# Kernel tuning notes

Hardware: AMD Instinct MI355X
Metric: run time of the kernel (lower is better)

## Reference

```python
import jax, jax.numpy as jnp
import numpy as np


def setup_inputs() -> dict:
    key = jax.random.key(0)
    ks = jax.random.split(key, 7)
    B, D, d1, d2, d3 = 256, 256, 1024, 512, 256
    s = lambda f: 1.0 / np.sqrt(f)  # torch nn.Linear-style init scale
    return {
        "x": jax.random.normal(ks[0], (B, D), jnp.float32),
        "W1": jax.random.normal(ks[1], (d1, D), jnp.float32) * s(D),
        "b1": jax.random.normal(ks[2], (d1,), jnp.float32) * s(D),
        "W2": jax.random.normal(ks[3], (d2, d1), jnp.float32) * s(d1),
        "b2": jax.random.normal(ks[4], (d2,), jnp.float32) * s(d1),
        "W3": jax.random.normal(ks[5], (d3, d2), jnp.float32) * s(d2),
        "b3": jax.random.normal(ks[6], (d3,), jnp.float32) * s(d2),
        "k": 10,
    }


def _border_dists(x, W1, b1, W2, b2, W3, b3):
    # Layer 1: pre-activations and boundary distances. For the first layer the
    # effective linear map is W1 itself (shared across the batch).
    z1 = x @ W1.T + b1                                   # [B, d1]
    dist1 = jnp.abs(z1) / jnp.linalg.norm(W1, axis=1)    # [B, d1]
    m1 = (z1 > 0).astype(x.dtype)
    V1 = m1[:, :, None] * W1[None]                       # [B, d1, D] per-instance map after ReLU
    h1 = m1 * z1

    # Layer 2
    z2 = h1 @ W2.T + b2                                  # [B, d2]
    V2 = jnp.einsum('oi,bid->bod', W2, V1)               # [B, d2, D]
    dist2 = jnp.abs(z2) / jnp.linalg.norm(V2, axis=2)
    m2 = (z2 > 0).astype(x.dtype)
    h2 = m2 * z2

    # Layer 3
    z3 = h2 @ W3.T + b3                                  # [B, d3]
    V3 = jnp.einsum('oi,bid->bod', W3, m2[:, :, None] * V2)  # [B, d3, D]
    dist3 = jnp.abs(z3) / jnp.linalg.norm(V3, axis=2)

    return jnp.concatenate([dist1, dist2, dist3], axis=1)  # [B, d1+d2+d3]


def reference(x, W1, b1, W2, b2, W3, b3, k):
    dists = _border_dists(x, W1, b1, W2, b2, W3, b3)
    # smallest-k distances per instance via top_k on negated distances
    neg_top, _ = jax.lax.top_k(-dists, k)                # [B, k]
    return jnp.sum(-neg_top)                             # border-distance loss (scalar)
```

## Files before the change

kernel.cpp:

```cpp
#include <hip/hip_runtime.h>
#include <math.h>
#include <float.h>

#define B   256
#define D   256
#define D1  1024
#define D2  512
#define D3  256
#define NDIST (D1 + D2 + D3)
#define CQ  2.0f

typedef __attribute__((ext_vector_type(8))) short short8;
typedef __attribute__((ext_vector_type(4))) float f32x4;
typedef __attribute__((ext_vector_type(4))) int   i32x4;

__device__ __forceinline__ float waveReduceSum(float v) {
    #pragma unroll
    for (int off = 32; off > 0; off >>= 1)
        v += __shfl_down(v, off, 64);
    return v;
}
__device__ __forceinline__ float waveReduceMax(float v) {
    #pragma unroll
    for (int off = 32; off > 0; off >>= 1)
        v = fmaxf(v, __shfl_down(v, off, 64));
    return v;
}
__device__ __forceinline__ unsigned short f2bf(float f) {
    unsigned int u = __float_as_uint(f);
    u = (u + 0x7FFFu + ((u >> 16) & 1u)) >> 16;
    return (unsigned short)u;
}
__device__ __forceinline__ float bf2f(unsigned short h) {
    return __uint_as_float(((unsigned int)h) << 16);
}
__device__ __forceinline__ void gld16(const void* g, void* l) {
    __builtin_amdgcn_global_load_lds(
        (const __attribute__((address_space(1))) unsigned int*)g,
        (__attribute__((address_space(3))) unsigned int*)l, 16, 0, 0);
}
__device__ __forceinline__ int swz_src(int row, int lane) {
    return ((lane & 3) + ((row >> 1) & 3)) & 3;
}
__device__ __forceinline__ int swz_frag(int row, int quad) {
    return row * 32 + (((quad - ((row >> 1) & 3)) & 3) * 8);
}

__device__ __forceinline__ void split_job(const float* src, unsigned short* hi,
                                          unsigned short* lo, int off) {
    float4 v = *(const float4*)(src + off);
    ushort4 h, l;
    h.x = f2bf(v.x); l.x = f2bf(v.x - bf2f(h.x));
    h.y = f2bf(v.y); l.y = f2bf(v.y - bf2f(h.y));
    h.z = f2bf(v.z); l.z = f2bf(v.z - bf2f(h.z));
    h.w = f2bf(v.w); l.w = f2bf(v.w - bf2f(h.w));
    *(ushort4*)(hi + off) = h;
    *(ushort4*)(lo + off) = l;
}

__device__ __forceinline__ void split8(const float* p, short8& h8, short8& l8) {
    float4 a = *(const float4*)(p);
    float4 b = *(const float4*)(p + 4);
    float hv[8] = { a.x, a.y, a.z, a.w, b.x, b.y, b.z, b.w };
    #pragma unroll
    for (int q = 0; q < 8; q++) {
        unsigned short hh = f2bf(hv[q]);
        h8[q] = (short)hh;
        l8[q] = (short)f2bf(hv[q] - bf2f(hh));
    }
}

template <int KD, int KL>
__device__ __forceinline__ void mfma3_64(
    const unsigned short* __restrict__ Ahi, const unsigned short* __restrict__ Alo,
    const unsigned short* __restrict__ Bhi, const unsigned short* __restrict__ Blo,
    int m0, int n0, int k0, unsigned short* sm, f32x4 acc[2][2]) {
    int tid = threadIdx.x;
    int l = tid & 63, w = tid >> 6;
    int rsub = l >> 2;
    int quad = l >> 4, l16 = l & 15;
    int wm = (w >> 1) * 32, wn = (w & 1) * 32;
    unsigned short* sAh = sm;
    unsigned short* sAl = sm + 2048;
    unsigned short* sBh = sm + 4096;
    unsigned short* sBl = sm + 6144;
    ptrdiff_t dA = Alo - Ahi, dB = Blo - Bhi;
    int rloc = w * 16 + rsub;
    int c = swz_src(rloc, l);
    const unsigned short* pa = Ahi + (size_t)(m0 + rloc) * KD + k0 + c * 8;
    const unsigned short* pb = Bhi + (size_t)(n0 + rloc) * KD + k0 + c * 8;
    int aoff[2], boff[2];
    #pragma unroll
    for (int mt = 0; mt < 2; mt++) aoff[mt] = swz_frag(wm + mt * 16 + l16, quad);
    #pragma unroll
    for (int nt = 0; nt < 2; nt++) boff[nt] = swz_frag(wn + nt * 16 + l16, quad);
    for (int kk = 0; kk < KL; kk += 32) {
        gld16(pa + kk,      sAh + w * 512);
        gld16(pa + dA + kk, sAl + w * 512);
        gld16(pb + kk,      sBh + w * 512);
        gld16(pb + dB + kk, sBl + w * 512);
        __syncthreads();
        short8 ah[2], al[2], bh[2], bl[2];
        #pragma unroll
        for (int mt = 0; mt < 2; mt++) {
            ah[mt] = *(const short8*)(sAh + aoff[mt]);
            al[mt] = *(const short8*)(sAl + aoff[mt]);
        }
        #pragma unroll
        for (int nt = 0; nt < 2; nt++) {
            bh[nt] = *(const short8*)(sBh + boff[nt]);
            bl[nt] = *(const short8*)(sBl + boff[nt]);
        }
        #pragma unroll
        for (int mt = 0; mt < 2; mt++)
            #pragma unroll
            for (int nt = 0; nt < 2; nt++) {
                acc[mt][nt] = __builtin_amdgcn_mfma_f32_16x16x32_bf16(ah[mt], bh[nt], acc[mt][nt], 0, 0, 0);
                acc[mt][nt] = __builtin_amdgcn_mfma_f32_16x16x32_bf16(ah[mt], bl[nt], acc[mt][nt], 0, 0, 0);
                acc[mt][nt] = __builtin_amdgcn_mfma_f32_16x16x32_bf16(al[mt], bh[nt], acc[mt][nt], 0, 0, 0);
            }
        __syncthreads();
    }
}

__global__ __launch_bounds__(256) void k_l1p(
    const float* __restrict__ x, const float* __restrict__ W1,
    const float* __restrict__ W2, const float* __restrict__ W3,
    const float* __restrict__ b1,
    float* __restrict__ dists, unsigned char* __restrict__ m1q,
    unsigned short* __restrict__ h1hi, unsigned short* __restrict__ h1lo,
    float* __restrict__ zeros, float* __restrict__ outp,
    unsigned short* __restrict__ W2hi, unsigned short* __restrict__ W2lo,
    unsigned short* __restrict__ W3hi, unsigned short* __restrict__ W3lo,
    signed char* __restrict__ W1Ti8, float* __restrict__ saq,
    signed char* __restrict__ W2i8,  float* __restrict__ sbq,
    signed char* __restrict__ W3i8,  float* __restrict__ s3q,
    float* __restrict__ rn1) {
    __shared__ __align__(16) unsigned short sm[8192];
    int blk = blockIdx.x;
    int t = threadIdx.x;

    if (blk < 64) {
        unsigned short* sAh = sm;
        unsigned short* sAl = sm + 2048;
        unsigned short* sBh = sm + 4096;
        unsigned short* sBl = sm + 6144;
        int m0 = (blk & 3) * 64, n0 = (blk >> 2) * 64;
        int l = t & 63, w = t >> 6;
        int rsub = l >> 2;
        int quad = l >> 4, l16 = l & 15;
        int wm = (w >> 1) * 32, wn = (w & 1) * 32;
        int rloc = w * 16 + rsub;
        int c = swz_src(rloc, l);
        const float* pax = x + (size_t)(m0 + rloc) * D + c * 8;
        const float* pbw = W1 + (size_t)(n0 + rloc) * D + c * 8;
        int aoff[2], boff[2];
        #pragma unroll
        for (int mt = 0; mt < 2; mt++) aoff[mt] = swz_frag(wm + mt * 16 + l16, quad);
        #pragma unroll
        for (int nt = 0; nt < 2; nt++) boff[nt] = swz_frag(wn + nt * 16 + l16, quad);
        int wrA = w * 512 + l * 8;
        f32x4 acc[2][2] = {};
        for (int kk = 0; kk < D; kk += 32) {
            short8 ha, la, hb, lb;
            split8(pax + kk, ha, la);
            split8(pbw + kk, hb, lb);
            *(short8*)(sAh + wrA) = ha;
            *(short8*)(sAl + wrA) = la;
            *(short8*)(sBh + wrA) = hb;
            *(short8*)(sBl + wrA) = lb;
            __syncthreads();
            short8 ah[2], al[2], bh[2], bl[2];
            #pragma unroll
            for (int mt = 0; mt < 2; mt++) {
                ah[mt] = *(const short8*)(sAh + aoff[mt]);
                al[mt] = *(const short8*)(sAl + aoff[mt]);
            }
            #pragma unroll
            for (int nt = 0; nt < 2; nt++) {
                bh[nt] = *(const short8*)(sBh + boff[nt]);
                bl[nt] = *(const short8*)(sBl + boff[nt]);
            }
            #pragma unroll
            for (int mt = 0; mt < 2; mt++)
                #pragma unroll
                for (int nt = 0; nt < 2; nt++) {
                    acc[mt][nt] = __builtin_amdgcn_mfma_f32_16x16x32_bf16(ah[mt], bh[nt], acc[mt][nt], 0, 0, 0);
                    acc[mt][nt] = __builtin_amdgcn_mfma_f32_16x16x32_bf16(ah[mt], bl[nt], acc[mt][nt], 0, 0, 0);
                    acc[mt][nt] = __builtin_amdgcn_mfma_f32_16x16x32_bf16(al[mt], bh[nt], acc[mt][nt], 0, 0, 0);
                }
            __syncthreads();
        }
        #pragma unroll
        for (int mt = 0; mt < 2; mt++)
            #pragma unroll
            for (int nt = 0; nt < 2; nt++) {
                int n = n0 + wn + nt * 16 + l16;
                float bv = b1[n];
                #pragma unroll
                for (int r = 0; r < 4; r++) {
                    int m = m0 + wm + mt * 16 + quad * 4 + r;
                    float z = acc[mt][nt][r] + bv;
                    size_t idx = (size_t)m * D1 + n;
                    dists[idx] = fabsf(z);
                    m1q[idx] = (z > 0.f) ? 0xFFu : 0u;
                    float h = z > 0.f ? z : 0.f;
                    unsigned short hh = f2bf(h);
                    h1hi[idx] = hh;
                    h1lo[idx] = f2bf(h - bf2f(hh));
                }
            }
        return;
    }
    if (blk < 448) {
        if (blk == 64 && t == 0) outp[0] = 0.f;
        int i4 = (blk - 64) * 1024 + t * 4;
        *(float4*)(zeros + i4) = make_float4(0.f, 0.f, 0.f, 0.f);
        return;
    }
    if (blk < 960) {
        split_job(W2, W2hi, W2lo, (blk - 448) * 1024 + t * 4);
        return;
    }
    if (blk < 1088) {
        split_job(W3, W3hi, W3lo, (blk - 960) * 1024 + t * 4);
        return;
    }
    if (blk < 1120) {
        int ty = t >> 5, tx = t & 31;
        int d = (blk - 1088) * 8 + ty;
        float m = 0.f;
        for (int i = tx; i < D1; i += 32) m = fmaxf(m, fabsf(W1[(size_t)i * D + d]));
        #pragma unroll
        for (int off = 16; off > 0; off >>= 1) m = fmaxf(m, __shfl_down(m, off, 32));
        m = __shfl(m, 0, 32);
        m = fmaxf(m, 1e-20f);
        if (tx == 0) saq[d] = m / 127.f;
        float inv = 127.f / m;
        for (int i = tx; i < D1; i += 32) {
            int q = __float2int_rn(W1[(size_t)i * D + d] * inv);
            W1Ti8[(size_t)d * D1 + i] = (signed char)q;
        }
        return;
    }
    if (blk < 1248) {
        int o = (blk - 1120) * 4 + (t >> 6);
        int l = t & 63;
        const float* row = W2 + (size_t)o * D1;
        float m = 0.f;
        for (int tt = l; tt < D1; tt += 64) m = fmaxf(m, fabsf(row[tt]));
        m = waveReduceMax(m);
        m = __shfl(m, 0, 64);
        m = fmaxf(m, 1e-20f);
        if (l == 0) sbq[o] = m / 127.f;
        float inv = 127.f / m;
        for (int tt = l; tt < D1; tt += 64)
            W2i8[(size_t)o * D1 + tt] = (signed char)__float2int_rn(row[tt] * inv);
        return;
    }
    if (blk < 1312) {
        int p = (blk - 1248) * 4 + (t >> 6);
        int l = t & 63;
        const float* row = W3 + (size_t)p * D2;
        float m = 0.f;
        for (int tt = l; tt < D2; tt += 64) m = fmaxf(m, fabsf(row[tt]));
        m = waveReduceMax(m);
        m = __shfl(m, 0, 64);
        m = fmaxf(m, 1e-20f);
        if (l == 0) s3q[p] = m / 127.f;
        float inv = 127.f / m;
        for (int tt = l; tt < D2; tt += 64)
            W3i8[(size_t)p * D2 + tt] = (signed char)__float2int_rn(row[tt] * inv);
        return;
    }
    {
        int gw = (blk - 1312) * 4 + (t >> 6);
        int lane = t & 63;
        const float* row = W1 + (size_t)gw * D;
        float s = 0.f;
        for (int tt = lane; tt < D; tt += 64) { float v = row[tt]; s += v * v; }
        s = waveReduceSum(s);
        if (lane == 0) rn1[gw] = sqrtf(s);
    }
}

__global__ __launch_bounds__(256, 2) void k_big1(
    const unsigned short* __restrict__ h1hi, const unsigned short* __restrict__ h1lo,
    const unsigned short* __restrict__ W2hi, const unsigned short* __restrict__ W2lo,
    float* __restrict__ z2,
    const signed char* __restrict__ W1Ti8,
    const signed char* __restrict__ W2i8,
    const unsigned char* __restrict__ m1q,
    const float* __restrict__ saq,
    const float* __restrict__ sbq,
    signed char* __restrict__ qV2,
    float* __restrict__ norm2) {
    __shared__ __align__(16) unsigned char smem[67584];
    int bid = blockIdx.x;

    if (bid < 128) {
        unsigned short* sm = (unsigned short*)smem;
        int m0 = (bid & 3) * 64, n0 = ((bid >> 2) & 7) * 64, k0 = (bid >> 5) * 256;
        f32x4 acc[2][2] = {};
        mfma3_64<D1, 256>(h1hi, h1lo, W2hi, W2lo, m0, n0, k0, sm, acc);
        int l = threadIdx.x & 63, w = threadIdx.x >> 6;
        int quad = l >> 4, l16 = l & 15;
        int wm = (w >> 1) * 32, wn = (w & 1) * 32;
        #pragma unroll
        for (int mt = 0; mt < 2; mt++)
            #pragma unroll
            for (int nt = 0; nt < 2; nt++) {
                int n = n0 + wn + nt * 16 + l16;
                #pragma unroll
                for (int r = 0; r < 4; r++) {
                    int m = m0 + wm + mt * 16 + quad * 4 + r;
                    atomicAdd(&z2[(size_t)m * D2 + n], acc[mt][nt][r]);
                }
            }
        return;
    }

    int j = bid - 128;
    int m0 = (j & 1) * 128;
    int o0 = ((j >> 1) & 3) * 128;
    int b0 = (j >> 3) * 2;
    int tid = threadIdx.x;
    int l = tid & 63, w = tid >> 6;
    int quad = l >> 4, l16 = l & 15;
    int wm = (w >> 1) * 64, wn = (w & 1) * 64;
    unsigned char* mbuf = (unsigned char*)smem + 65536;

    *(int2*)(mbuf + tid * 8) = *(const int2*)(m1q + (size_t)b0 * D1 + tid * 8);

    const signed char* pa[4];
    const signed char* pb[4];
    int lrow = l >> 3, ls = l & 7;
    #pragma unroll
    for (int r = 0; r < 4; r++) {
        int row = r * 32 + w * 8 + lrow;
        int c = (ls + (row & 7)) & 7;
        pa[r] = W1Ti8 + (size_t)(m0 + row) * D1 + c * 16;
        pb[r] = W2i8 + (size_t)(o0 + row) * D1 + c * 16;
    }
    int aoff[4][2], boff[4][2];
    #pragma unroll
    for (int mt = 0; mt < 4; mt++) {
        int tr = wm + mt * 16 + l16;
        #pragma unroll
        for (int ks = 0; ks < 2; ks++)
            aoff[mt][ks] = tr * 128 + (((ks * 4 + quad) - (tr & 7)) & 7) * 16;
    }
    #pragma unroll
    for (int nt = 0; nt < 4; nt++) {
        int tr = wn + nt * 16 + l16;
        #pragma unroll
        for (int ks = 0; ks < 2; ks++)
            boff[nt][ks] = tr * 128 + (((ks * 4 + quad) - (tr & 7)) & 7) * 16;
    }

    i32x4 acc[2][4][4];
    #pragma unroll
    for (int g = 0; g < 2; g++)
        #pragma unroll
        for (int i = 0; i < 4; i++)
            #pragma unroll
            for (int jj = 0; jj < 4; jj++) acc[g][i][jj] = (i32x4)0;

    {
        signed char* buf0 = (signed char*)smem;
        #pragma unroll
        for (int r = 0; r < 4; r++) {
            gld16(pa[r], buf0 + r * 4096 + w * 1024);
            gld16(pb[r], buf0 + 16384 + r * 4096 + w * 1024);
        }
    }
    __syncthreads();

    #pragma unroll
    for (int t = 0; t < 8; t++) {
        signed char* bufc = (signed char*)smem + ((t & 1) << 15);
        signed char* bufn = (signed char*)smem + (((t + 1) & 1) << 15);
        if (t < 7) {
            int kn = (t + 1) * 128;
            #pragma unroll
            for (int r = 0; r < 4; r++) {
                gld16(pa[r] + kn, bufn + r * 4096 + w * 1024);
                gld16(pb[r] + kn, bufn + 16384 + r * 4096 + w * 1024);
            }
        }
        const signed char* As = bufc;
        const signed char* Bs = bufc + 16384;
        #pragma unroll
        for (int ks = 0; ks < 2; ks++) {
            i32x4 mva = *(const i32x4*)(mbuf +        t * 128 + ks * 64 + quad * 16);
            i32x4 mvb = *(const i32x4*)(mbuf + 1024 + t * 128 + ks * 64 + quad * 16);
            i32x4 a[4], bq[4];
            #pragma unroll
            for (int mt = 0; mt < 4; mt++)
                a[mt] = *(const i32x4*)(As + aoff[mt][ks]);
            #pragma unroll
            for (int nt = 0; nt < 4; nt++)
                bq[nt] = *(const i32x4*)(Bs + boff[nt][ks]);
            #pragma unroll
            for (int mt = 0; mt < 4; mt++) {
                i32x4 a0 = a[mt] & mva;
                i32x4 a1 = a[mt] & mvb;
                #pragma unroll
                for (int nt = 0; nt < 4; nt++)
                    acc[0][mt][nt] = __builtin_amdgcn_mfma_i32_16x16x64_i8(
                        a0, bq[nt], acc[0][mt][nt], 0, 0, 0);
                #pragma unroll
                for (int nt = 0; nt < 4; nt++)
                    acc[1][mt][nt] = __builtin_amdgcn_mfma_i32_16x16x64_i8(
                        a1, bq[nt], acc[1][mt][nt], 0, 0, 0);
            }
        }
        __syncthreads();
    }

    float sad[4][4];
    #pragma unroll
    for (int mt = 0; mt < 4; mt++)
        #pragma unroll
        for (int r = 0; r < 4; r++)
            sad[mt][r] = saq[m0 + wm + mt * 16 + quad * 4 + r];
    float sbv[4], sbdq[4];
    #pragma unroll
    for (int nt = 0; nt < 4; nt++) {
        sbv[nt] = sbq[o0 + wn + nt * 16 + l16];
        sbdq[nt] = sbv[nt] * (1.0f / CQ);
    }

    #pragma unroll
    for (int g = 0; g < 2; g++) {
        int bg = b0 + g;
        float nrm[4] = {0.f, 0.f, 0.f, 0.f};
        signed char* qb = qV2 + (size_t)bg * (D * D2);
        #pragma unroll
        for (int mt = 0; mt < 4; mt++) {
            int dbase = m0 + wm + mt * 16 + quad * 4;
            #pragma unroll
            for (int r = 0; r < 4; r++) {
                float sa = sad[mt][r];
                size_t rowoff = (size_t)(dbase + r) * D2;
                #pragma unroll
                for (int nt = 0; nt < 4; nt++) {
                    float tv = (float)acc[g][mt][nt][r];
                    float u = tv * sa;
                    nrm[nt] = fmaf(u, u, nrm[nt]);
                    int qi = __float2int_rn(tv * sbdq[nt]);
                    qi = max(-127, min(127, qi));
                    qb[rowoff + o0 + wn + nt * 16 + l16] = (signed char)qi;
                }
            }
        }
        #pragma unroll
        for (int nt = 0; nt < 4; nt++) {
            float s = nrm[nt] * (sbv[nt] * sbv[nt]);
            s += __shfl_down(s, 32, 64);
            s += __shfl_down(s, 16, 64);
            if (l < 16)
                atomicAdd(&norm2[(size_t)bg * D2 + o0 + wn + nt * 16 + l], s);
        }
    }
}

__global__ __launch_bounds__(256) void k_big2(
    const float* __restrict__ z2,
    const float* __restrict__ b2,
    const unsigned short* __restrict__ W3hi, const unsigned short* __restrict__ W3lo,
    float* __restrict__ z3,
    const signed char* __restrict__ W3i8,
    const signed char* __restrict__ qV2,
    const float* __restrict__ saq,
    const float* __restrict__ s3q,
    float* __restrict__ norm3) {
    __shared__ __align__(16) unsigned char smem[33280];
    int bid = blockIdx.x;
    int tid = threadIdx.x;

    if (bid < 32) {
        unsigned short* sAh = (unsigned short*)smem;
        unsigned short* sAl = sAh + 2048;
        unsigned short* sBh = sAh + 4096;
        unsigned short* sBl = sAh + 6144;
        int m0 = (bid & 3) * 64, n0 = ((bid >> 2) & 3) * 64, k0 = (bid >> 4) * 256;
        int l = tid & 63, w = tid >> 6;
        int rsub = l >> 2;
        int quad = l >> 4, l16 = l & 15;
        int wm = (w >> 1) * 32, wn = (w & 1) * 32;
        int rloc = w * 16 + rsub;
        int c = swz_src(rloc, l);
        const float* pz  = z2 + (size_t)(m0 + rloc) * D2 + k0 + c * 8;
        const float* pbi = b2 + k0 + c * 8;
        const unsigned short* pb = W3hi + (size_t)(n0 + rloc) * D2 + k0 + c * 8;
        ptrdiff_t dB = W3lo - W3hi;
        int aoff[2], boff[2];
        #pragma unroll
        for (int mt = 0; mt < 2; mt++) aoff[mt] = swz_frag(wm + mt * 16 + l16, quad);
        #pragma unroll
        for (int nt = 0; nt < 2; nt++) boff[nt] = swz_frag(wn + nt * 16 + l16, quad);
        int wrA = w * 512 + l * 8;
        f32x4 acc[2][2] = {};
        for (int kk = 0; kk < 256; kk += 32) {
            gld16(pb + kk,      sBh + w * 512);
            gld16(pb + dB + kk, sBl + w * 512);
            float4 za = *(const float4*)(pz + kk);
            float4 zb = *(const float4*)(pz + kk + 4);
            float4 ba = *(const float4*)(pbi + kk);
            float4 bb = *(const float4*)(pbi + kk + 4);
            float hv[8] = { za.x + ba.x, za.y + ba.y, za.z + ba.z, za.w + ba.w,
                            zb.x + bb.x, zb.y + bb.y, zb.z + bb.z, zb.w + bb.w };
            short8 h8, l8;
            #pragma unroll
            for (int q2 = 0; q2 < 8; q2++) {
                float h = hv[q2] > 0.f ? hv[q2] : 0.f;
                unsigned short hh = f2bf(h);
                h8[q2] = (short)hh;
                l8[q2] = (short)f2bf(h - bf2f(hh));
            }
            *(short8*)(sAh + wrA) = h8;
            *(short8*)(sAl + wrA) = l8;
            __syncthreads();
            short8 ah[2], al[2], bh[2], bl[2];
            #pragma unroll
            for (int mt = 0; mt < 2; mt++) {
                ah[mt] = *(const short8*)(sAh + aoff[mt]);
                al[mt] = *(const short8*)(sAl + aoff[mt]);
            }
            #pragma unroll
            for (int nt = 0; nt < 2; nt++) {
                bh[nt] = *(const short8*)(sBh + boff[nt]);
                bl[nt] = *(const short8*)(sBl + boff[nt]);
            }
            #pragma unroll
            for (int mt = 0; mt < 2; mt++)
                #pragma unroll
                for (int nt = 0; nt < 2; nt++) {
                    acc[mt][nt] = __builtin_amdgcn_mfma_f32_16x16x32_bf16(ah[mt], bh[nt], acc[mt][nt], 0, 0, 0);
                    acc[mt][nt] = __builtin_amdgcn_mfma_f32_16x16x32_bf16(ah[mt], bl[nt], acc[mt][nt], 0, 0, 0);
                    acc[mt][nt] = __builtin_amdgcn_mfma_f32_16x16x32_bf16(al[mt], bh[nt], acc[mt][nt], 0, 0, 0);
                }
            __syncthreads();
        }
        #pragma unroll
        for (int mt = 0; mt < 2; mt++)
            #pragma unroll
            for (int nt = 0; nt < 2; nt++) {
                int n = n0 + wn + nt * 16 + l16;
                #pragma unroll
                for (int r = 0; r < 4; r++) {
                    int m = m0 + wm + mt * 16 + quad * 4 + r;
                    atomicAdd(&z3[(size_t)m * D3 + n], acc[mt][nt][r]);
                }
            }
        return;
    }

    int j = bid - 32;
    signed char* As = (signed char*)smem;
    signed char* Bs = (signed char*)smem + 16384;
    unsigned char* mbuf = (unsigned char*)smem + 32768;
    int m0 = (j & 1) * 128;
    int n0 = ((j >> 1) & 1) * 128;
    int bc = j >> 2;
    int l = tid & 63, w = tid >> 6;
    int quad = l >> 4, l16 = l & 15;
    int wm = (w >> 1) * 64, wn = (w & 1) * 64;
    const signed char* Bsrc = qV2 + (size_t)bc * (D * D2);

    {
        #pragma unroll
        for (int rr = 0; rr < 2; rr++) {
            int o = tid * 2 + rr;
            float z = z2[(size_t)bc * D2 + o] + b2[o];
            mbuf[o] = (z > 0.f) ? 0xFFu : 0u;
        }
    }
    __syncthreads();

    const signed char* pa[4];
    const signed char* pb[4];
    int lrow = l >> 3, ls = l & 7;
    #pragma unroll
    for (int r = 0; r < 4; r++) {
        int row = r * 32 + w * 8 + lrow;
        int c = (ls + (row & 7)) & 7;
        pa[r] = W3i8 + (size_t)(m0 + row) * D2 + c * 16;
        pb[r] = Bsrc + (size_t)(n0 + row) * D2 + c * 16;
    }
    int aoff[4][2], boff[4][2];
    #pragma unroll
    for (int mt = 0; mt < 4; mt++) {
        int tr = wm + mt * 16 + l16;
        #pragma unroll
        for (int ks = 0; ks < 2; ks++)
            aoff[mt][ks] = tr * 128 + (((ks * 4 + quad) - (tr & 7)) & 7) * 16;
    }
    #pragma unroll
    for (int nt = 0; nt < 4; nt++) {
        int tr = wn + nt * 16 + l16;
        #pragma unroll
        for (int ks = 0; ks < 2; ks++)
            boff[nt][ks] = tr * 128 + (((ks * 4 + quad) - (tr & 7)) & 7) * 16;
    }

    i32x4 acc[4][4];
    #pragma unroll
    for (int i = 0; i < 4; i++)
        #pragma unroll
        for (int jj = 0; jj < 4; jj++) acc[i][jj] = (i32x4)0;

    for (int kk = 0; kk < D2; kk += 128) {
        #pragma unroll
        for (int r = 0; r < 4; r++) {
            gld16(pa[r] + kk, As + r * 4096 + w * 1024);
            gld16(pb[r] + kk, Bs + r * 4096 + w * 1024);
        }
        __syncthreads();
        i32x4 mv0 = *(const i32x4*)(mbuf + kk + quad * 16);
        i32x4 mv1 = *(const i32x4*)(mbuf + kk + 64 + quad * 16);
        #pragma unroll
        for (int ks = 0; ks < 2; ks++) {
            i32x4 mv = ks ? mv1 : mv0;
            i32x4 a[4], bq[4];
            #pragma unroll
            for (int mt = 0; mt < 4; mt++)
                a[mt] = *(const i32x4*)(As + aoff[mt][ks]);
            #pragma unroll
            for (int nt = 0; nt < 4; nt++)
                bq[nt] = (*(const i32x4*)(Bs + boff[nt][ks])) & mv;
            #pragma unroll
            for (int mt = 0; mt < 4; mt++)
                #pragma unroll
                for (int nt = 0; nt < 4; nt++)
                    acc[mt][nt] = __builtin_amdgcn_mfma_i32_16x16x64_i8(
                        a[mt], bq[nt], acc[mt][nt], 0, 0, 0);
        }
        __syncthreads();
    }

    float saCQ[4];
    #pragma unroll
    for (int nt = 0; nt < 4; nt++)
        saCQ[nt] = saq[n0 + wn + nt * 16 + l16] * CQ;

    #pragma unroll
    for (int mt = 0; mt < 4; mt++)
        #pragma unroll
        for (int r = 0; r < 4; r++) {
            float s = 0.f;
            #pragma unroll
            for (int nt = 0; nt < 4; nt++) {
                float v = (float)acc[mt][nt][r] * saCQ[nt];
                s += v * v;
            }
            s += __shfl_down(s, 8, 64);
            s += __shfl_down(s, 4, 64);
            s += __shfl_down(s, 2, 64);
            s += __shfl_down(s, 1, 64);
            if (l16 == 0) {
                int p = m0 + wm + mt * 16 + quad * 4 + r;
                float s3 = s3q[p];
                atomicAdd(&norm3[(size_t)bc * D3 + p], s * s3 * s3);
            }
        }
}

__global__ __launch_bounds__(256) void k_topk(
    const float* __restrict__ dists,
    const float* __restrict__ rn1,
    const float* __restrict__ z2, const float* __restrict__ b2,
    const float* __restrict__ norm2,
    const float* __restrict__ z3, const float* __restrict__ b3,
    const float* __restrict__ norm3,
    const int* __restrict__ kp, float* __restrict__ outp) {
    int t = threadIdx.x;
    int wv = t >> 6, lane = t & 63;
    int b = blockIdx.x * 4 + wv;
    float lv[28];
    #pragma unroll
    for (int j = 0; j < 16; j++) {
        int n = lane + 64 * j;
        lv[j] = dists[(size_t)b * D1 + n] / rn1[n];
    }
    #pragma unroll
    for (int j = 16; j < 24; j++) {
        int o = lane + 64 * (j - 16);
        float zz = z2[(size_t)b * D2 + o] + b2[o];
        lv[j] = fabsf(zz) / sqrtf(norm2[(size_t)b * D2 + o]);
    }
    #pragma unroll
    for (int j = 24; j < 28; j++) {
        int p = lane + 64 * (j - 24);
        float zz = z3[(size_t)b * D3 + p] + b3[p];
        lv[j] = fabsf(zz) / sqrtf(norm3[(size_t)b * D3 + p]);
    }
    int k = *kp;
    if (k > NDIST) k = NDIST;
    float sum = 0.f;
    for (int it = 0; it < k; it++) {
        float mv = lv[0]; int mj = 0;
        #pragma unroll
        for (int j = 1; j < 28; j++)
            if (lv[j] < mv) { mv = lv[j]; mj = j; }
        unsigned long long key =
            ((unsigned long long)__float_as_uint(mv) << 32) | (unsigned)(lane * 32 + mj);
        #pragma unroll
        for (int off = 1; off < 64; off <<= 1) {
            unsigned long long o = __shfl_xor(key, off, 64);
            if (o < key) key = o;
        }
        sum += __uint_as_float((unsigned)(key >> 32));
        int wl = (int)((key >> 5) & 63u), wj = (int)(key & 31u);
        if (lane == wl) lv[wj] = FLT_MAX;
    }
    if (lane == 0) atomicAdd(outp, sum);
}

extern "C" void kernel_launch(void* const* d_in, const int* in_sizes, int n_in,
                              void* d_out, int out_size, void* d_ws, size_t ws_size,
                              hipStream_t stream) {
    const float* x  = (const float*)d_in[0];
    const float* W1 = (const float*)d_in[1];
    const float* b1 = (const float*)d_in[2];
    const float* W2 = (const float*)d_in[3];
    const float* b2 = (const float*)d_in[4];
    const float* W3 = (const float*)d_in[5];
    const float* b3 = (const float*)d_in[6];
    const int*   kp = (const int*)d_in[7];
    float* outp = (float*)d_out;

    float* fp = (float*)d_ws;
    float* rn1     = fp;                          fp += D1;
    float* dists   = fp;                          fp += (size_t)B * D1;
    float* saq     = fp;                          fp += D;
    float* sbq     = fp;                          fp += D2;
    float* s3q     = fp;                          fp += D3;
    float* z2      = fp;                          fp += (size_t)B * D2;
    float* z3      = fp;                          fp += (size_t)B * D3;
    float* norm2   = fp;                          fp += (size_t)B * D2;
    float* norm3   = fp;                          fp += (size_t)B * D3;
    unsigned short* up = (unsigned short*)fp;
    unsigned short* W2hi  = up;  up += (size_t)D2 * D1;
    unsigned short* W2lo  = up;  up += (size_t)D2 * D1;
    unsigned short* W3hi  = up;  up += (size_t)D3 * D2;
    unsigned short* W3lo  = up;  up += (size_t)D3 * D2;
    unsigned short* h1hi  = up;  up += (size_t)B * D1;
    unsigned short* h1lo  = up;  up += (size_t)B * D1;
    signed char*    cp = (signed char*)up;
    signed char*    W1Ti8 = cp;  cp += (size_t)D * D1;
    signed char*    W2i8  = cp;  cp += (size_t)D2 * D1;
    signed char*    W3i8  = cp;  cp += (size_t)D3 * D2;
    unsigned char*  m1q   = (unsigned char*)cp;  cp += (size_t)B * D1;
    signed char*    qV2   = cp;

    k_l1p<<<1568, 256, 0, stream>>>(x, W1, W2, W3, b1,
                                    dists, m1q, h1hi, h1lo,
                                    z2, outp, W2hi, W2lo, W3hi, W3lo,
                                    W1Ti8, saq, W2i8, sbq, W3i8, s3q, rn1);

    k_big1<<<1152, 256, 0, stream>>>(h1hi, h1lo, W2hi, W2lo, z2,
                                     W1Ti8, W2i8, m1q, saq, sbq, qV2, norm2);

    k_big2<<<1056, 256, 0, stream>>>(z2, b2, W3hi, W3lo, z3,
                                     W3i8, qV2, saq, s3q, norm3);

    k_topk<<<B / 4, 256, 0, stream>>>(dists, rn1, z2, b2, norm2, z3, b3, norm3,
                                      kp, outp);
}
```

Before: 160.9 us.

## Fuse weight split/quantize jobs and register-staged double-buffer int8 GEMMs

The prep kernel now handles the bf16 hi/lo split of W2 and W3 in the same blocks that quantize them to int8. Each row is read once as float4 and the packed int8 is written with a single 32-bit store, which removes the separate split blocks and shrinks the grid. In k_big1 and k_big2, the async global-to-LDS loads are replaced by loads into registers that are written to LDS after the MFMA work. k_big2 also gains a double buffer with one fewer barrier per step, so the next tile's loads overlap compute. The cost is more registers, and doubled shared memory in k_big2 (about 66 KB), which may limit occupancy despite launch_bounds(256,2).

```diff
diff --git a/kernel.cpp b/kernel.cpp
--- a/kernel.cpp
+++ b/kernel.cpp
@@ -44,18 +44,6 @@
 }
 __device__ __forceinline__ int swz_frag(int row, int quad) {
     return row * 32 + (((quad - ((row >> 1) & 3)) & 3) * 8);
-}
-
-__device__ __forceinline__ void split_job(const float* src, unsigned short* hi,
-                                          unsigned short* lo, int off) {
-    float4 v = *(const float4*)(src + off);
-    ushort4 h, l;
-    h.x = f2bf(v.x); l.x = f2bf(v.x - bf2f(h.x));
-    h.y = f2bf(v.y); l.y = f2bf(v.y - bf2f(h.y));
-    h.z = f2bf(v.z); l.z = f2bf(v.z - bf2f(h.z));
-    h.w = f2bf(v.w); l.w = f2bf(v.w - bf2f(h.w));
-    *(ushort4*)(hi + off) = h;
-    *(ushort4*)(lo + off) = l;
 }
 
 __device__ __forceinline__ void split8(const float* p, short8& h8, short8& l8) {
@@ -218,17 +206,9 @@
         *(float4*)(zeros + i4) = make_float4(0.f, 0.f, 0.f, 0.f);
         return;
     }
-    if (blk < 960) {
-        split_job(W2, W2hi, W2lo, (blk - 448) * 1024 + t * 4);
-        return;
-    }
-    if (blk < 1088) {
-        split_job(W3, W3hi, W3lo, (blk - 960) * 1024 + t * 4);
-        return;
-    }
-    if (blk < 1120) {
+    if (blk < 480) {
         int ty = t >> 5, tx = t & 31;
-        int d = (blk - 1088) * 8 + ty;
+        int d = (blk - 448) * 8 + ty;
         float m = 0.f;
         for (int i = tx; i < D1; i += 32) m = fmaxf(m, fabsf(W1[(size_t)i * D + d]));
         #pragma unroll
@@ -243,38 +223,82 @@
         }
         return;
     }
-    if (blk < 1248) {
-        int o = (blk - 1120) * 4 + (t >> 6);
+    if (blk < 608) {
+        int o = (blk - 480) * 4 + (t >> 6);
         int l = t & 63;
         const float* row = W2 + (size_t)o * D1;
+        float4 v[4];
+        #pragma unroll
+        for (int jj = 0; jj < 4; jj++) v[jj] = *(const float4*)(row + jj * 256 + l * 4);
         float m = 0.f;
-        for (int tt = l; tt < D1; tt += 64) m = fmaxf(m, fabsf(row[tt]));
+        #pragma unroll
+        for (int jj = 0; jj < 4; jj++)
+            m = fmaxf(m, fmaxf(fmaxf(fabsf(v[jj].x), fabsf(v[jj].y)),
+                               fmaxf(fabsf(v[jj].z), fabsf(v[jj].w))));
         m = waveReduceMax(m);
         m = __shfl(m, 0, 64);
         m = fmaxf(m, 1e-20f);
         if (l == 0) sbq[o] = m / 127.f;
         float inv = 127.f / m;
-        for (int tt = l; tt < D1; tt += 64)
-            W2i8[(size_t)o * D1 + tt] = (signed char)__float2int_rn(row[tt] * inv);
+        #pragma unroll
+        for (int jj = 0; jj < 4; jj++) {
+            int base = jj * 256 + l * 4;
+            int q0 = __float2int_rn(v[jj].x * inv);
+            int q1 = __float2int_rn(v[jj].y * inv);
+            int q2 = __float2int_rn(v[jj].z * inv);
+            int q3 = __float2int_rn(v[jj].w * inv);
+            unsigned int pk = (unsigned)(q0 & 255) | ((unsigned)(q1 & 255) << 8) |
+                              ((unsigned)(q2 & 255) << 16) | ((unsigned)(q3 & 255) << 24);
+            *(unsigned int*)(W2i8 + (size_t)o * D1 + base) = pk;
+            ushort4 h, lo;
+            h.x = f2bf(v[jj].x); lo.x = f2bf(v[jj].x - bf2f(h.x));
+            h.y = f2bf(v[jj].y); lo.y = f2bf(v[jj].y - bf2f(h.y));
+            h.z = f2bf(v[jj].z); lo.z = f2bf(v[jj].z - bf2f(h.z));
+            h.w = f2bf(v[jj].w); lo.w = f2bf(v[jj].w - bf2f(h.w));
+            *(ushort4*)(W2hi + (size_t)o * D1 + base) = h;
+            *(ushort4*)(W2lo + (size_t)o * D1 + base) = lo;
+        }
         return;
     }
-    if (blk < 1312) {
-        int p = (blk - 1248) * 4 + (t >> 6);
+    if (blk < 672) {
+        int p = (blk - 608) * 4 + (t >> 6);
         int l = t & 63;
         const float* row = W3 + (size_t)p * D2;
+        float4 v[2];
+        #pragma unroll
+        for (int jj = 0; jj < 2; jj++) v[jj] = *(const float4*)(row + jj * 256 + l * 4);
         float m = 0.f;
-        for (int tt = l; tt < D2; tt += 64) m = fmaxf(m, fabsf(row[tt]));
+        #pragma unroll
+        for (int jj = 0; jj < 2; jj++)
+            m = fmaxf(m, fmaxf(fmaxf(fabsf(v[jj].x), fabsf(v[jj].y)),
+                               fmaxf(fabsf(v[jj].z), fabsf(v[jj].w))));
         m = waveReduceMax(m);
         m = __shfl(m, 0, 64);
         m = fmaxf(m, 1e-20f);
         if (l == 0) s3q[p] = m / 127.f;
         float inv = 127.f / m;
-        for (int tt = l; tt < D2; tt += 64)
-            W3i8[(size_t)p * D2 + tt] = (signed char)__float2int_rn(row[tt] * inv);
+        #pragma unroll
+        for (int jj = 0; jj < 2; jj++) {
+            int base = jj * 256 + l * 4;
+            int q0 = __float2int_rn(v[jj].x * inv);
+            int q1 = __float2int_rn(v[jj].y * inv);
+            int q2 = __float2int_rn(v[jj].z * inv);
+            int q3 = __float2int_rn(v[jj].w * inv);
+            unsigned int pk = (unsigned)(q0 & 255) | ((unsigned)(q1 & 255) << 8) |
+                              ((unsigned)(q2 & 255) << 16) | ((unsigned)(q3 & 255) << 24);
+            *(unsigned int*)(W3i8 + (size_t)p * D2 + base) = pk;
+            ushort4 h, lo;
+            h.x = f2bf(v[jj].x); lo.x = f2bf(v[jj].x - bf2f(h.x));
+            h.y = f2bf(v[jj].y); lo.y = f2bf(v[jj].y - bf2f(h.y));
+            h.z = f2bf(v[jj].z); lo.z = f2bf(v[jj].z - bf2f(h.z));
+            h.w = f2bf(v[jj].w); lo.w = f2bf(v[jj].w - bf2f(h.w));
+            *(ushort4*)(W3hi + (size_t)p * D2 + base) = h;
+            *(ushort4*)(W3lo + (size_t)p * D2 + base) = lo;
+        }
         return;
     }
     {
-        int gw = (blk - 1312) * 4 + (t >> 6);
+        int gw = (blk - 672) * 4 + (t >> 6);
         int lane = t & 63;
         const float* row = W1 + (size_t)gw * D;
         float s = 0.f;
@@ -366,26 +390,33 @@
             #pragma unroll
             for (int jj = 0; jj < 4; jj++) acc[g][i][jj] = (i32x4)0;
 
+    int wr = w * 1024 + l * 16;
+    i32x4 sga[4], sgb[4];
+    #pragma unroll
+    for (int r = 0; r < 4; r++) {
+        sga[r] = *(const i32x4*)(pa[r]);
+        sgb[r] = *(const i32x4*)(pb[r]);
+    }
     {
         signed char* buf0 = (signed char*)smem;
         #pragma unroll
         for (int r = 0; r < 4; r++) {
-            gld16(pa[r], buf0 + r * 4096 + w * 1024);
-            gld16(pb[r], buf0 + 16384 + r * 4096 + w * 1024);
+            *(i32x4*)(buf0 + r * 4096 + wr) = sga[r];
+            *(i32x4*)(buf0 + 16384 + r * 4096 + wr) = sgb[r];
         }
     }
     __syncthreads();
 
     #pragma unroll
     for (int t = 0; t < 8; t++) {
-        signed char* bufc = (signed char*)smem + ((t & 1) << 15);
+        const signed char* bufc = (const signed char*)smem + ((t & 1) << 15);
         signed char* bufn = (signed char*)smem + (((t + 1) & 1) << 15);
         if (t < 7) {
             int kn = (t + 1) * 128;
             #pragma unroll
             for (int r = 0; r < 4; r++) {
-                gld16(pa[r] + kn, bufn + r * 4096 + w * 1024);
-                gld16(pb[r] + kn, bufn + 16384 + r * 4096 + w * 1024);
+                sga[r] = *(const i32x4*)(pa[r] + kn);
+                sgb[r] = *(const i32x4*)(pb[r] + kn);
             }
         }
         const signed char* As = bufc;
@@ -413,6 +444,13 @@
                 for (int nt = 0; nt < 4; nt++)
                     acc[1][mt][nt] = __builtin_amdgcn_mfma_i32_16x16x64_i8(
                         a1, bq[nt], acc[1][mt][nt], 0, 0, 0);
+            }
+        }
+        if (t < 7) {
+            #pragma unroll
+            for (int r = 0; r < 4; r++) {
+                *(i32x4*)(bufn + r * 4096 + wr) = sga[r];
+                *(i32x4*)(bufn + 16384 + r * 4096 + wr) = sgb[r];
             }
         }
         __syncthreads();
@@ -465,7 +503,7 @@
     }
 }
 
-__global__ __launch_bounds__(256) void k_big2(
+__global__ __launch_bounds__(256, 2) void k_big2(
     const float* __restrict__ z2,
     const float* __restrict__ b2,
     const unsigned short* __restrict__ W3hi, const unsigned short* __restrict__ W3lo,
@@ -475,7 +513,7 @@
     const float* __restrict__ saq,
     const float* __restrict__ s3q,
     float* __restrict__ norm3) {
-    __shared__ __align__(16) unsigned char smem[33280];
+    __shared__ __align__(16) unsigned char smem[66048];
     int bid = blockIdx.x;
     int tid = threadIdx.x;
 
@@ -558,9 +596,7 @@
     }
 
     int j = bid - 32;
-    signed char* As = (signed char*)smem;
-    signed char* Bs = (signed char*)smem + 16384;
-    unsigned char* mbuf = (unsigned char*)smem + 32768;
+    unsigned char* mbuf = (unsigned char*)smem + 65536;
     int m0 = (j & 1) * 128;
     int n0 = ((j >> 1) & 1) * 128;
     int bc = j >> 2;
@@ -577,7 +613,6 @@
             mbuf[o] = (z > 0.f) ? 0xFFu : 0u;
         }
     }
-    __syncthreads();
 
     const signed char* pa[4];
     const signed char* pb[4];
@@ -611,13 +646,38 @@
         #pragma unroll
         for (int jj = 0; jj < 4; jj++) acc[i][jj] = (i32x4)0;
 
-    for (int kk = 0; kk < D2; kk += 128) {
+    int wr = w * 1024 + l * 16;
+    i32x4 sga[4], sgb[4];
+    #pragma unroll
+    for (int r = 0; r < 4; r++) {
+        sga[r] = *(const i32x4*)(pa[r]);
+        sgb[r] = *(const i32x4*)(pb[r]);
+    }
+    {
+        signed char* buf0 = (signed char*)smem;
         #pragma unroll
         for (int r = 0; r < 4; r++) {
-            gld16(pa[r] + kk, As + r * 4096 + w * 1024);
-            gld16(pb[r] + kk, Bs + r * 4096 + w * 1024);
-        }
-        __syncthreads();
+            *(i32x4*)(buf0 + r * 4096 + wr) = sga[r];
+            *(i32x4*)(buf0 + 16384 + r * 4096 + wr) = sgb[r];
+        }
+    }
+    __syncthreads();
+
+    #pragma unroll
+    for (int t = 0; t < 4; t++) {
+        const signed char* bufc = (const signed char*)smem + ((t & 1) << 15);
+        signed char* bufn = (signed char*)smem + (((t + 1) & 1) << 15);
+        if (t < 3) {
+            int kn = (t + 1) * 128;
+            #pragma unroll
+            for (int r = 0; r < 4; r++) {
+                sga[r] = *(const i32x4*)(pa[r] + kn);
+                sgb[r] = *(const i32x4*)(pb[r] + kn);
+            }
+        }
+        int kk = t * 128;
+        const signed char* As = bufc;
+        const signed char* Bs = bufc + 16384;
         i32x4 mv0 = *(const i32x4*)(mbuf + kk + quad * 16);
         i32x4 mv1 = *(const i32x4*)(mbuf + kk + 64 + quad * 16);
         #pragma unroll
@@ -636,6 +696,13 @@
                 for (int nt = 0; nt < 4; nt++)
                     acc[mt][nt] = __builtin_amdgcn_mfma_i32_16x16x64_i8(
                         a[mt], bq[nt], acc[mt][nt], 0, 0, 0);
+        }
+        if (t < 3) {
+            #pragma unroll
+            for (int r = 0; r < 4; r++) {
+                *(i32x4*)(bufn + r * 4096 + wr) = sga[r];
+                *(i32x4*)(bufn + 16384 + r * 4096 + wr) = sgb[r];
+            }
         }
         __syncthreads();
     }
@@ -755,10 +822,10 @@
     unsigned char*  m1q   = (unsigned char*)cp;  cp += (size_t)B * D1;
     signed char*    qV2   = cp;
 
-    k_l1p<<<1568, 256, 0, stream>>>(x, W1, W2, W3, b1,
-                                    dists, m1q, h1hi, h1lo,
-                                    z2, outp, W2hi, W2lo, W3hi, W3lo,
-                                    W1Ti8, saq, W2i8, sbq, W3i8, s3q, rn1);
+    k_l1p<<<928, 256, 0, stream>>>(x, W1, W2, W3, b1,
+                                   dists, m1q, h1hi, h1lo,
+                                   z2, outp, W2hi, W2lo, W3hi, W3lo,
+                                   W1Ti8, saq, W2i8, sbq, W3i8, s3q, rn1);
 
     k_big1<<<1152, 256, 0, stream>>>(h1hi, h1lo, W2hi, W2lo, z2,
                                      W1Ti8, W2i8, m1q, saq, sbq, qV2, norm2);
```

Measured after the change: 170.9 us. 6.2% more time.
